# Performance work log

Hardware: AMD Instinct MI355X
Metric: run time of the kernel (lower is better)

Reference implementation:

```python
import jax, jax.numpy as jnp
import numpy as np

B, T = 128, 2048
O, E, L = 128, 512, 34  # o_size, embed_dim, num_letter


def setup_inputs() -> dict:
    key = jax.random.key(0)
    ks = jax.random.split(key, 16)
    u = lambda k, shape, s: jax.random.uniform(k, shape, jnp.float32, -s, s)
    hk = jax.random.normal(ks[0], (B, T, O), jnp.float32)
    hv = jax.random.normal(ks[1], (B, T, O), jnp.float32)
    y_1 = jax.random.normal(ks[2], (B, E), jnp.float32)
    c_1 = jax.random.normal(ks[3], (B, O), jnp.float32)
    sh_1 = jax.random.normal(ks[4], (B, O), jnp.float32)
    sc_1 = jax.random.normal(ks[5], (B, O), jnp.float32)
    # valid-length mask (each row has at least T//2 valid positions)
    lengths = jax.random.randint(ks[6], (B,), T // 2, T + 1)
    mask = (jnp.arange(T)[None, :] < lengths[:, None]).astype(jnp.float32)
    s_rnn = 1.0 / np.sqrt(O)
    W_ih = u(ks[7], (4 * O, O + E), s_rnn)
    b_ih = u(ks[8], (4 * O,), s_rnn)
    W_hh = u(ks[9], (4 * O, O), s_rnn)
    b_hh = u(ks[10], (4 * O,), s_rnn)
    s1 = 1.0 / np.sqrt(O)
    W1 = u(ks[11], (L, O), s1); b1 = u(ks[12], (L,), s1)
    W2 = u(ks[13], (L, O), s1); b2 = u(ks[14], (L,), s1)
    s3 = 1.0 / np.sqrt(L)
    W3 = u(ks[15], (L, L), s3); b3 = u(jax.random.fold_in(key, 99), (L,), s3)
    return {"hk": hk, "hv": hv, "y_1": y_1, "c_1": c_1, "sh_1": sh_1,
            "sc_1": sc_1, "mask": mask, "W_ih": W_ih, "b_ih": b_ih,
            "W_hh": W_hh, "b_hh": b_hh, "W1": W1, "b1": b1,
            "W2": W2, "b2": b2, "W3": W3, "b3": b3}


def reference(hk, hv, y_1, c_1, sh_1, sc_1, mask,
              W_ih, b_ih, W_hh, b_hh, W1, b1, W2, b2, W3, b3):
    # LSTMCell (PyTorch gate order: i, f, g, o)
    x = jnp.concatenate([y_1, c_1], axis=1)            # [B, O+E]
    gates = x @ W_ih.T + b_ih + sh_1 @ W_hh.T + b_hh   # [B, 4O]
    i, f, g, o = jnp.split(gates, 4, axis=1)
    sc = jax.nn.sigmoid(f) * sc_1 + jax.nn.sigmoid(i) * jnp.tanh(g)
    sh = jax.nn.sigmoid(o) * jnp.tanh(sc)
    # attention scores keyed on cell state sc (faithful to source)
    scores = jnp.einsum('bto,bo->bt', hk, sc)          # [B, T]
    attn = jax.nn.softmax(scores, axis=1) * mask
    attn = attn / jnp.sum(attn, axis=1, keepdims=True)
    c = jnp.einsum('bt,bto->bo', attn, hv)             # [B, O]
    out = jax.nn.relu(sh @ W1.T + b1 + c @ W2.T + b2)
    out = jax.nn.softmax(out @ W3.T + b3, axis=1)      # [B, L]
    return (out, c, sh, sc)
```

## Files before the change

### kernel.cpp

```cpp
#include <hip/hip_runtime.h>
#include <math.h>

#define BB 128
#define TT 2048
#define OO 128
#define EE 512
#define LL 34
#define XDIM 640
#define SUBCH 64
#define SUB_LEN 32

__device__ __forceinline__ float sigmoidf_(float x) { return 1.0f / (1.0f + __expf(-x)); }

__global__ __launch_bounds__(256) void lstm_kernel(
    const float* __restrict__ y1, const float* __restrict__ c1,
    const float* __restrict__ sh1, const float* __restrict__ sc1,
    const float* __restrict__ Wih, const float* __restrict__ bih,
    const float* __restrict__ Whh, const float* __restrict__ bhh,
    float* __restrict__ out_sh, float* __restrict__ out_sc)
{
    __shared__ float xs[4][768];
    __shared__ float gbuf[4][4][16];
    const int tid = threadIdx.x;
    const int otile = blockIdx.x;
    const int qb = blockIdx.y * 4;

    for (int idx = tid; idx < 4 * 768; idx += 256) {
        int bi = idx / 768, k = idx - bi * 768;
        int b = qb + bi;
        float v;
        if (k < 512)      v = y1[b * EE + k];
        else if (k < 640) v = c1[b * OO + (k - 512)];
        else              v = sh1[b * OO + (k - 640)];
        xs[bi][k] = v;
    }
    __syncthreads();

    const int g = tid >> 6, l = tid & 63;
    #pragma unroll 2
    for (int i = 0; i < 16; ++i) {
        const int row = g * 128 + otile * 16 + i;
        const float* wr = Wih + (size_t)row * XDIM;
        float a0 = 0.f, a1 = 0.f, a2 = 0.f, a3 = 0.f;
        #pragma unroll
        for (int j = 0; j < 10; ++j) {
            float wv = wr[l + 64 * j];
            a0 += wv * xs[0][l + 64 * j];
            a1 += wv * xs[1][l + 64 * j];
            a2 += wv * xs[2][l + 64 * j];
            a3 += wv * xs[3][l + 64 * j];
        }
        const float* wh = Whh + (size_t)row * OO;
        #pragma unroll
        for (int j = 0; j < 2; ++j) {
            float wv = wh[l + 64 * j];
            a0 += wv * xs[0][640 + l + 64 * j];
            a1 += wv * xs[1][640 + l + 64 * j];
            a2 += wv * xs[2][640 + l + 64 * j];
            a3 += wv * xs[3][640 + l + 64 * j];
        }
        #pragma unroll
        for (int off = 32; off >= 1; off >>= 1) {
            a0 += __shfl_xor(a0, off);
            a1 += __shfl_xor(a1, off);
            a2 += __shfl_xor(a2, off);
            a3 += __shfl_xor(a3, off);
        }
        if (l == 0) {
            float bb = bih[row] + bhh[row];
            gbuf[g][0][i] = a0 + bb;
            gbuf[g][1][i] = a1 + bb;
            gbuf[g][2][i] = a2 + bb;
            gbuf[g][3][i] = a3 + bb;
        }
    }
    __syncthreads();

    if (tid < 64) {
        const int bi = tid >> 4, ol = tid & 15;
        const int b = qb + bi, o = otile * 16 + ol;
        float gi = gbuf[0][bi][ol], gf = gbuf[1][bi][ol];
        float gg = gbuf[2][bi][ol], go = gbuf[3][bi][ol];
        float sc = sigmoidf_(gf) * sc1[b * OO + o] + sigmoidf_(gi) * tanhf(gg);
        float sh = sigmoidf_(go) * tanhf(sc);
        out_sc[b * OO + o] = sc;
        out_sh[b * OO + o] = sh;
    }
}

__global__ __launch_bounds__(256) void attn_kernel(
    const float* __restrict__ hk, const float* __restrict__ hv,
    const float* __restrict__ mask, const float* __restrict__ sc,
    float* __restrict__ ws_c, float2* __restrict__ pbuf)
{
    const int b = blockIdx.y;
    const int tid = threadIdx.x;
    const int wave = tid >> 6, lane = tid & 63;
    const int subchunk = blockIdx.x * 4 + wave;
    const int sg = (lane >> 4) & 3, l = lane & 15;
    const int r0 = subchunk * SUB_LEN;

    const float4 scA = *(const float4*)(sc + b * OO + l * 8);
    const float4 scB = *(const float4*)(sc + b * OO + l * 8 + 4);
    const float* krow = hk + ((size_t)b * TT + r0 + sg * 8) * OO;
    const float* mrow = mask + (size_t)b * TT + r0 + sg * 8;

    float s[8];
    bool val[8];
    #pragma unroll
    for (int i = 0; i < 8; ++i) {
        val[i] = (mrow[i] != 0.f);
        float4 a  = *(const float4*)(krow + (size_t)i * OO + l * 8);
        float4 c2 = *(const float4*)(krow + (size_t)i * OO + l * 8 + 4);
        s[i] = a.x * scA.x + a.y * scA.y + a.z * scA.z + a.w * scA.w
             + c2.x * scB.x + c2.y * scB.y + c2.z * scB.z + c2.w * scB.w;
    }
    #pragma unroll
    for (int i = 0; i < 8; ++i) {
        s[i] += __shfl_xor(s[i], 8);
        s[i] += __shfl_xor(s[i], 4);
        s[i] += __shfl_xor(s[i], 2);
        s[i] += __shfl_xor(s[i], 1);
    }
    float m = -INFINITY;
    #pragma unroll
    for (int i = 0; i < 8; ++i) if (val[i]) m = fmaxf(m, s[i]);
    m = fmaxf(m, __shfl_xor(m, 16));
    m = fmaxf(m, __shfl_xor(m, 32));

    float e[8];
    float ps = 0.f;
    #pragma unroll
    for (int i = 0; i < 8; ++i) {
        e[i] = val[i] ? __expf(s[i] - m) : 0.f;
        ps += e[i];
    }
    ps += __shfl_xor(ps, 16);
    ps += __shfl_xor(ps, 32);
    if (lane == 0)
        pbuf[(size_t)b * SUBCH + subchunk] = make_float2(m, ps);

    const int c4 = (lane & 31) * 4, rp = lane >> 5;
    float4 acc = make_float4(0.f, 0.f, 0.f, 0.f);
    if (ps > 0.f) {
        const float* vbase = hv + ((size_t)b * TT + r0) * OO + c4;
        #pragma unroll
        for (int sgi = 0; sgi < 4; ++sgi) {
            float wv[8];
            #pragma unroll
            for (int i = 0; i < 8; ++i) wv[i] = __shfl(e[i], sgi * 16);
            #pragma unroll
            for (int j = 0; j < 4; ++j) {
                const int row = sgi * 8 + j * 2 + rp;
                float4 v = *(const float4*)(vbase + (size_t)row * OO);
                float w = (rp == 0) ? wv[2 * j] : wv[2 * j + 1];
                acc.x += w * v.x;
                acc.y += w * v.y;
                acc.z += w * v.z;
                acc.w += w * v.w;
            }
        }
    }
    acc.x += __shfl_xor(acc.x, 32);
    acc.y += __shfl_xor(acc.y, 32);
    acc.z += __shfl_xor(acc.z, 32);
    acc.w += __shfl_xor(acc.w, 32);
    if (rp == 0)
        *(float4*)(ws_c + ((size_t)b * SUBCH + subchunk) * OO + c4) = acc;
}

__global__ __launch_bounds__(256) void final_kernel(
    const float* __restrict__ ws_c, const float2* __restrict__ pbuf,
    const float* __restrict__ sh_in,
    const float* __restrict__ W1, const float* __restrict__ b1,
    const float* __restrict__ W2, const float* __restrict__ b2,
    const float* __restrict__ W3, const float* __restrict__ b3,
    float* __restrict__ out_p, float* __restrict__ out_c)
{
    const int b = blockIdx.x, tid = threadIdx.x;
    __shared__ float marr[SUBCH], Sarr[SUBCH], fac[SUBCH];
    __shared__ float cbuf[128], shbuf[128], h1[LL], zz[LL], red2[2];

    if (tid < SUBCH) {
        float2 p = pbuf[(size_t)b * SUBCH + tid];
        marr[tid] = p.x;
        Sarr[tid] = p.y;
    }
    __syncthreads();
    if (tid < SUBCH) {
        float M = marr[0];
        #pragma unroll
        for (int i = 1; i < SUBCH; ++i) M = fmaxf(M, marr[i]);
        float S = 0.f;
        #pragma unroll
        for (int i = 0; i < SUBCH; ++i) S += Sarr[i] * __expf(marr[i] - M);
        fac[tid] = __expf(marr[tid] - M) / S;
    }
    __syncthreads();

    if (tid < 128) {
        float s = 0.f;
        const float* base = ws_c + (size_t)b * SUBCH * OO + tid;
        #pragma unroll 8
        for (int i = 0; i < SUBCH; ++i) s += fac[i] * base[i * OO];
        cbuf[tid] = s;
        out_c[b * OO + tid] = s;
        shbuf[tid] = sh_in[b * OO + tid];
    }
    __syncthreads();

    const int o = tid >> 2, l2 = tid & 3;
    if (o < LL) {
        float a = 0.f;
        const float* w1r = W1 + o * OO;
        const float* w2r = W2 + o * OO;
        #pragma unroll 8
        for (int j = 0; j < 32; ++j) {
            int k = l2 + 4 * j;
            a += w1r[k] * shbuf[k] + w2r[k] * cbuf[k];
        }
        a += __shfl_xor(a, 1);
        a += __shfl_xor(a, 2);
        if (l2 == 0) h1[o] = fmaxf(a + b1[o] + b2[o], 0.f);
    }
    __syncthreads();

    if (o < LL) {
        float z = 0.f;
        const float* w3r = W3 + o * LL;
        for (int j = 0; j < 9; ++j) {
            int k = l2 + 4 * j;
            if (k < LL) z += w3r[k] * h1[k];
        }
        z += __shfl_xor(z, 1);
        z += __shfl_xor(z, 2);
        if (l2 == 0) zz[o] = z + b3[o];
    }
    __syncthreads();
    if (tid == 0) {
        float mm = zz[0];
        for (int i = 1; i < LL; i++) mm = fmaxf(mm, zz[i]);
        float ss = 0.f;
        for (int i = 0; i < LL; i++) ss += __expf(zz[i] - mm);
        red2[0] = mm; red2[1] = ss;
    }
    __syncthreads();
    if (tid < LL) out_p[b * LL + tid] = __expf(zz[tid] - red2[0]) / red2[1];
}

extern "C" void kernel_launch(void* const* d_in, const int* in_sizes, int n_in,
                              void* d_out, int out_size, void* d_ws, size_t ws_size,
                              hipStream_t stream) {
    (void)in_sizes; (void)n_in; (void)out_size; (void)ws_size;
    const float* hk   = (const float*)d_in[0];
    const float* hv   = (const float*)d_in[1];
    const float* y1   = (const float*)d_in[2];
    const float* c1   = (const float*)d_in[3];
    const float* sh1  = (const float*)d_in[4];
    const float* sc1  = (const float*)d_in[5];
    const float* mask = (const float*)d_in[6];
    const float* Wih  = (const float*)d_in[7];
    const float* bih  = (const float*)d_in[8];
    const float* Whh  = (const float*)d_in[9];
    const float* bhh  = (const float*)d_in[10];
    const float* W1   = (const float*)d_in[11];
    const float* b1   = (const float*)d_in[12];
    const float* W2   = (const float*)d_in[13];
    const float* b2   = (const float*)d_in[14];
    const float* W3   = (const float*)d_in[15];
    const float* b3   = (const float*)d_in[16];

    float* out    = (float*)d_out;
    float* out_c  = out + BB * LL;
    float* out_sh = out_c + BB * OO;
    float* out_sc = out_sh + BB * OO;

    float*  ws_c = (float*)d_ws;
    float2* pbuf = (float2*)(ws_c + (size_t)BB * SUBCH * OO);

    lstm_kernel<<<dim3(8, 32), 256, 0, stream>>>(y1, c1, sh1, sc1, Wih, bih, Whh, bhh,
                                                 out_sh, out_sc);
    attn_kernel<<<dim3(SUBCH / 4, BB), 256, 0, stream>>>(hk, hv, mask, out_sc, ws_c, pbuf);
    final_kernel<<<BB, 256, 0, stream>>>(ws_c, pbuf, out_sh, W1, b1, W2, b2, W3, b3,
                                         out, out_c);
}
```

Before: 330.6 us.

## Restructure attention kernel to issue all K and V loads upfront per lane

Each lane now owns a fixed 4-column slice of 16 rows (two half-waves interleave rows) and loads all hk and hv rows into registers before any reductions. V loads are issued before the score shuffles and softmax, so the two memory streams overlap instead of V waiting on the scores. The old cross-lane weight broadcast is replaced by per-lane local FMAs. The early skip of V loads for fully masked subchunks is removed. It adds register pressure (about 128 floats for kv/vv), which the launch bound of 2 must accommodate.

```diff
diff --git a/kernel.cpp b/kernel.cpp
--- a/kernel.cpp
+++ b/kernel.cpp
@@ -88,7 +88,7 @@
     }
 }
 
-__global__ __launch_bounds__(256) void attn_kernel(
+__global__ __launch_bounds__(256, 2) void attn_kernel(
     const float* __restrict__ hk, const float* __restrict__ hv,
     const float* __restrict__ mask, const float* __restrict__ sc,
     float* __restrict__ ws_c, float2* __restrict__ pbuf)
@@ -97,76 +97,71 @@
     const int tid = threadIdx.x;
     const int wave = tid >> 6, lane = tid & 63;
     const int subchunk = blockIdx.x * 4 + wave;
-    const int sg = (lane >> 4) & 3, l = lane & 15;
+    const int p = lane >> 5, q = lane & 31;
     const int r0 = subchunk * SUB_LEN;
 
-    const float4 scA = *(const float4*)(sc + b * OO + l * 8);
-    const float4 scB = *(const float4*)(sc + b * OO + l * 8 + 4);
-    const float* krow = hk + ((size_t)b * TT + r0 + sg * 8) * OO;
-    const float* mrow = mask + (size_t)b * TT + r0 + sg * 8;
-
-    float s[8];
-    bool val[8];
-    #pragma unroll
-    for (int i = 0; i < 8; ++i) {
-        val[i] = (mrow[i] != 0.f);
-        float4 a  = *(const float4*)(krow + (size_t)i * OO + l * 8);
-        float4 c2 = *(const float4*)(krow + (size_t)i * OO + l * 8 + 4);
-        s[i] = a.x * scA.x + a.y * scA.y + a.z * scA.z + a.w * scA.w
-             + c2.x * scB.x + c2.y * scB.y + c2.z * scB.z + c2.w * scB.w;
-    }
-    #pragma unroll
-    for (int i = 0; i < 8; ++i) {
-        s[i] += __shfl_xor(s[i], 8);
-        s[i] += __shfl_xor(s[i], 4);
-        s[i] += __shfl_xor(s[i], 2);
-        s[i] += __shfl_xor(s[i], 1);
+    const float4 scq = *(const float4*)(sc + b * OO + q * 4);
+    const float* mbase = mask + (size_t)b * TT + r0 + p;
+    const float* kbase = hk + ((size_t)b * TT + r0 + p) * OO + q * 4;
+    const float* vbase = hv + ((size_t)b * TT + r0 + p) * OO + q * 4;
+
+    float mk[16];
+    #pragma unroll
+    for (int j = 0; j < 16; ++j) mk[j] = mbase[2 * j];
+
+    float4 kv[16];
+    #pragma unroll
+    for (int j = 0; j < 16; ++j)
+        kv[j] = *(const float4*)(kbase + (size_t)(2 * j) * OO);
+
+    float d[16];
+    #pragma unroll
+    for (int j = 0; j < 16; ++j)
+        d[j] = kv[j].x * scq.x + kv[j].y * scq.y + kv[j].z * scq.z + kv[j].w * scq.w;
+
+    float4 vv[16];
+    #pragma unroll
+    for (int j = 0; j < 16; ++j)
+        vv[j] = *(const float4*)(vbase + (size_t)(2 * j) * OO);
+
+    #pragma unroll
+    for (int j = 0; j < 16; ++j) {
+        d[j] += __shfl_xor(d[j], 1);
+        d[j] += __shfl_xor(d[j], 2);
+        d[j] += __shfl_xor(d[j], 4);
+        d[j] += __shfl_xor(d[j], 8);
+        d[j] += __shfl_xor(d[j], 16);
     }
     float m = -INFINITY;
     #pragma unroll
-    for (int i = 0; i < 8; ++i) if (val[i]) m = fmaxf(m, s[i]);
-    m = fmaxf(m, __shfl_xor(m, 16));
+    for (int j = 0; j < 16; ++j) if (mk[j] != 0.f) m = fmaxf(m, d[j]);
     m = fmaxf(m, __shfl_xor(m, 32));
 
-    float e[8];
+    float e[16];
     float ps = 0.f;
     #pragma unroll
-    for (int i = 0; i < 8; ++i) {
-        e[i] = val[i] ? __expf(s[i] - m) : 0.f;
-        ps += e[i];
-    }
-    ps += __shfl_xor(ps, 16);
+    for (int j = 0; j < 16; ++j) {
+        e[j] = (mk[j] != 0.f) ? __expf(d[j] - m) : 0.f;
+        ps += e[j];
+    }
     ps += __shfl_xor(ps, 32);
     if (lane == 0)
         pbuf[(size_t)b * SUBCH + subchunk] = make_float2(m, ps);
 
-    const int c4 = (lane & 31) * 4, rp = lane >> 5;
     float4 acc = make_float4(0.f, 0.f, 0.f, 0.f);
-    if (ps > 0.f) {
-        const float* vbase = hv + ((size_t)b * TT + r0) * OO + c4;
-        #pragma unroll
-        for (int sgi = 0; sgi < 4; ++sgi) {
-            float wv[8];
-            #pragma unroll
-            for (int i = 0; i < 8; ++i) wv[i] = __shfl(e[i], sgi * 16);
-            #pragma unroll
-            for (int j = 0; j < 4; ++j) {
-                const int row = sgi * 8 + j * 2 + rp;
-                float4 v = *(const float4*)(vbase + (size_t)row * OO);
-                float w = (rp == 0) ? wv[2 * j] : wv[2 * j + 1];
-                acc.x += w * v.x;
-                acc.y += w * v.y;
-                acc.z += w * v.z;
-                acc.w += w * v.w;
-            }
-        }
+    #pragma unroll
+    for (int j = 0; j < 16; ++j) {
+        acc.x += e[j] * vv[j].x;
+        acc.y += e[j] * vv[j].y;
+        acc.z += e[j] * vv[j].z;
+        acc.w += e[j] * vv[j].w;
     }
     acc.x += __shfl_xor(acc.x, 32);
     acc.y += __shfl_xor(acc.y, 32);
     acc.z += __shfl_xor(acc.z, 32);
     acc.w += __shfl_xor(acc.w, 32);
-    if (rp == 0)
-        *(float4*)(ws_c + ((size_t)b * SUBCH + subchunk) * OO + c4) = acc;
+    if (p == 0)
+        *(float4*)(ws_c + ((size_t)b * SUBCH + subchunk) * OO + q * 4) = acc;
 }
 
 __global__ __launch_bounds__(256) void final_kernel(
```

Result: slower. 337.8 us (+2.2%).
